# Performance work log

Measured on AMD Instinct MI355X. Metric: run time of the kernel, lower is better.

Reference implementation:

```python
import jax, jax.numpy as jnp
import numpy as np

LEAKY_SLOPE = 0.01

def bilinear_interpolate(grid, coords):
    # grid: [H, W, C]; coords: [N, 2] in [0,1] (x, y order as in torch code)
    H = grid.shape[0] - 1
    W = grid.shape[1] - 1
    fx = coords[:, 0] * W
    fy = coords[:, 1] * H
    x0 = fx.astype(jnp.int32)
    y0 = fy.astype(jnp.int32)
    xf = jnp.mod(fx, 1.0)
    yf = jnp.mod(fy, 1.0)
    x1 = jnp.minimum(x0 + 1, W)
    y1 = jnp.minimum(y0 + 1, H)
    tl = grid[y0, x0]  # [N, C]
    tr = grid[y0, x1]
    bl = grid[y1, x0]
    br = grid[y1, x1]
    xf = xf[:, None]
    yf = yf[:, None]
    top = (1.0 - xf) * tl + xf * tr
    bot = (1.0 - xf) * bl + xf * br
    return (1.0 - yf) * top + yf * bot


def setup_inputs() -> dict:
    key = jax.random.key(0)
    ks = jax.random.split(key, 10)
    N = 2097152
    pos = jax.random.uniform(ks[0], (N, 2), dtype=jnp.float32)
    dir = jax.random.uniform(ks[1], (N, 2), dtype=jnp.float32)
    pos_grid = jax.random.normal(ks[2], (256, 256, 3), dtype=jnp.float32) * 10.0
    dir_grid = jax.random.normal(ks[3], (256, 256, 3), dtype=jnp.float32) * 10.0
    # Linear layers: PyTorch default init U(-1/sqrt(fan_in), 1/sqrt(fan_in))
    def linear(kw, kb, fan_in, fan_out):
        bound = 1.0 / np.sqrt(fan_in)
        W = jax.random.uniform(kw, (fan_out, fan_in), minval=-bound, maxval=bound, dtype=jnp.float32)
        b = jax.random.uniform(kb, (fan_out,), minval=-bound, maxval=bound, dtype=jnp.float32)
        return W, b
    W1, b1 = linear(ks[4], ks[5], 6, 64)
    W2, b2 = linear(ks[6], ks[7], 64, 64)
    W3, b3 = linear(ks[8], ks[9], 64, 1)
    return {"pos": pos, "dir": dir, "pos_grid": pos_grid, "dir_grid": dir_grid,
            "W1": W1, "b1": b1, "W2": W2, "b2": b2, "W3": W3, "b3": b3}


def reference(pos, dir, pos_grid, dir_grid, W1, b1, W2, b2, W3, b3):
    pos_feat = jax.lax.stop_gradient(bilinear_interpolate(pos_grid, pos))  # .detach() in torch
    dir_feat = jax.lax.stop_gradient(bilinear_interpolate(dir_grid, dir))
    x = jnp.concatenate([pos_feat, dir_feat], axis=1)  # [N, 6]
    x = jax.nn.leaky_relu(x @ W1.T + b1, LEAKY_SLOPE)
    x = jax.nn.leaky_relu(x @ W2.T + b2, LEAKY_SLOPE)
    return jax.nn.sigmoid(x @ W3.T + b3)  # [N, 1]
```

## Files before the change

### kernel.cpp

```cpp
#include <hip/hip_runtime.h>
#include <hip/hip_bf16.h>
#include <math.h>


#define NTHREADS 256
#define NB 4
#define LSTRIDE 72
#define WAVE_L (64 * LSTRIDE)

typedef __attribute__((ext_vector_type(8))) short bf16x8;
typedef __attribute__((ext_vector_type(4))) float f32x4;
typedef __attribute__((ext_vector_type(4))) int i32x4;
typedef __attribute__((ext_vector_type(2))) int i32x2;

static __device__ __forceinline__ short f2bf(float f) {
    return __builtin_bit_cast(short, __float2bfloat16(f));
}
static __device__ __forceinline__ int pk2(float lo, float hi) {
    unsigned short l = (unsigned short)f2bf(lo);
    unsigned short h = (unsigned short)f2bf(hi);
    return (int)(((unsigned int)h << 16) | (unsigned int)l);
}
static __device__ __forceinline__ float bflo(int u) {
    return __builtin_bit_cast(float, u << 16);
}
static __device__ __forceinline__ float bfhi(int u) {
    return __builtin_bit_cast(float, (int)(u & 0xffff0000));
}

__global__ __launch_bounds__(256) void make_patches(
    const float* __restrict__ g, int* __restrict__ pout) {
    int id = blockIdx.x * 256 + threadIdx.x;
    int y0 = id >> 8, x0 = id & 255;
    int x1 = min(x0 + 1, 255), y1 = min(y0 + 1, 255);
    const float* tl = g + (y0 * 256 + x0) * 3;
    const float* tr = g + (y0 * 256 + x1) * 3;
    const float* bl = g + (y1 * 256 + x0) * 3;
    const float* br = g + (y1 * 256 + x1) * 3;
    i32x4 u0;
    i32x2 u1;
    u0[0] = pk2(tl[0], bl[0]);
    u0[1] = pk2(tl[1], bl[1]);
    u0[2] = pk2(tl[2], bl[2]);
    u0[3] = pk2(tr[0], br[0]);
    u1[0] = pk2(tr[1], br[1]);
    u1[1] = pk2(tr[2], br[2]);
    *(i32x4*)(pout + id * 8) = u0;
    *(i32x2*)(pout + id * 8 + 4) = u1;
}

static __device__ __forceinline__ void patch_issue(
    const int* __restrict__ tab, float px, float py, int* P, float& xf,
    float& yf) {
    float fx = px * 255.0f;
    float fy = py * 255.0f;
    int x0 = (int)fx;
    int y0 = (int)fy;
    xf = fx - floorf(fx);
    yf = fy - floorf(fy);
    int idx = (y0 << 8) | x0;
    i32x4 a = *(const i32x4*)(tab + idx * 8);
    i32x2 b = *(const i32x2*)(tab + idx * 8 + 4);
    P[0] = a[0]; P[1] = a[1]; P[2] = a[2];
    P[3] = a[3]; P[4] = b[0]; P[5] = b[1];
}

static __device__ __forceinline__ void patch_lerp(const int* P, float xf,
                                                  float yf, float* f) {
#pragma unroll
    for (int ch = 0; ch < 3; ++ch) {
        float tl = bflo(P[ch]), bl = bfhi(P[ch]);
        float tr = bflo(P[ch + 3]), br = bfhi(P[ch + 3]);
        float top = fmaf(xf, tr - tl, tl);
        float bot = fmaf(xf, br - bl, bl);
        f[ch] = fmaf(yf, bot - top, top);
    }
}

__global__ __launch_bounds__(NTHREADS, 3) void mlp_mfma_kernel(
    const float* __restrict__ pos, const float* __restrict__ dir,
    const int* __restrict__ patP, const int* __restrict__ patD,
    const float* __restrict__ W1, const float* __restrict__ b1,
    const float* __restrict__ W2, const float* __restrict__ b2,
    const float* __restrict__ W3, const float* __restrict__ b3,
    float* __restrict__ out) {
    __shared__ short lds_L[4 * WAVE_L];
    __shared__ int lds_F[4 * 2 * 64 * 4];

    const int w = threadIdx.x >> 6;
    const int lane = threadIdx.x & 63;
    const int c = lane & 15;
    const int q = lane >> 4;

    short* L = lds_L + w * WAVE_L;
    int* FB = lds_F + w * (2 * 64 * 4);

    bf16x8 A1f[4];
#pragma unroll
    for (int mt = 0; mt < 4; ++mt) {
        int f = mt * 16 + c;
        bf16x8 t;
#pragma unroll
        for (int j = 0; j < 8; ++j) {
            float v = 0.0f;
            if (q == 0) {
                if (j < 6) v = W1[f * 6 + j];
                else if (j == 6) v = b1[f];
            }
            t[j] = f2bf(v);
        }
        A1f[mt] = t;
    }
    bf16x8 A2f[2][4];
#pragma unroll
    for (int kt = 0; kt < 2; ++kt)
#pragma unroll
        for (int mt = 0; mt < 4; ++mt) {
            int n2 = mt * 16 + c;
            int k0 = kt * 32 + q * 8;
            bf16x8 t;
#pragma unroll
            for (int j = 0; j < 8; ++j) t[j] = f2bf(W2[n2 * 64 + k0 + j]);
            A2f[kt][mt] = t;
        }
    f32x4 ci[4], w3q[4];
#pragma unroll
    for (int ft = 0; ft < 4; ++ft)
#pragma unroll
        for (int r = 0; r < 4; ++r) {
            ci[ft][r] = b2[ft * 16 + q * 4 + r];
            w3q[ft][r] = W3[ft * 16 + q * 4 + r];
        }
    const float b3s = b3[0];
    const int dbias = pk2(1.0f, 0.0f);

    const long wave_global = (long)blockIdx.x * 4 + w;
    const long base0 = wave_global * (64L * NB);
    const f32x4 zacc = {0.f, 0.f, 0.f, 0.f};
    const float2* pos2 = (const float2*)pos;
    const float2* dir2 = (const float2*)dir;

    int PA[12], PB[12];
    float frA[4], frB[4];
    float2 cp2, cd2, cp3, cd3;

    {
        float2 c0p = pos2[base0 + lane], c0d = dir2[base0 + lane];
        float2 c1p = pos2[base0 + 64 + lane], c1d = dir2[base0 + 64 + lane];
        cp2 = pos2[base0 + 128 + lane];
        cd2 = dir2[base0 + 128 + lane];
        cp3 = pos2[base0 + 192 + lane];
        cd3 = dir2[base0 + 192 + lane];
        int P0_[12];
        float fr0[4];
        patch_issue(patP, c0p.x, c0p.y, P0_, fr0[0], fr0[1]);
        patch_issue(patD, c0d.x, c0d.y, P0_ + 6, fr0[2], fr0[3]);
        float feat[6];
        patch_lerp(P0_, fr0[0], fr0[1], feat);
        patch_lerp(P0_ + 6, fr0[2], fr0[3], feat + 3);
        i32x4 dv;
        dv[0] = pk2(feat[0], feat[1]);
        dv[1] = pk2(feat[2], feat[3]);
        dv[2] = pk2(feat[4], feat[5]);
        dv[3] = dbias;
        *(i32x4*)(FB + lane * 4) = dv;
        patch_issue(patP, c1p.x, c1p.y, PA, frA[0], frA[1]);
        patch_issue(patD, c1d.x, c1d.y, PA + 6, frA[2], frA[3]);
    }

#pragma unroll 1
    for (int ib = 0; ib < NB; ++ib) {
        const long base = base0 + ib * 64;
        const int cur = ib & 1;

        patch_issue(patP, cp2.x, cp2.y, PB, frB[0], frB[1]);
        patch_issue(patD, cd2.x, cd2.y, PB + 6, frB[2], frB[3]);

        {
            float feat[6];
            patch_lerp(PA, frA[0], frA[1], feat);
            patch_lerp(PA + 6, frA[2], frA[3], feat + 3);
            i32x4 dv;
            dv[0] = pk2(feat[0], feat[1]);
            dv[1] = pk2(feat[2], feat[3]);
            dv[2] = pk2(feat[4], feat[5]);
            dv[3] = dbias;
            *(i32x4*)(FB + (cur ^ 1) * 256 + lane * 4) = dv;
        }

#pragma unroll
        for (int pt = 0; pt < 4; ++pt) {
            const int row = pt * 16 + c;
            i32x4 bi = *(const i32x4*)(FB + cur * 256 + row * 4);
            bf16x8 bfrag = __builtin_bit_cast(bf16x8, bi);
            f32x4 a1[4];
#pragma unroll
            for (int mt = 0; mt < 4; ++mt)
                a1[mt] = __builtin_amdgcn_mfma_f32_16x16x32_bf16(
                    A1f[mt], bfrag, zacc, 0, 0, 0);
#pragma unroll
            for (int mt = 0; mt < 4; ++mt) {
                float l0 = a1[mt][0], l1 = a1[mt][1];
                float l2 = a1[mt][2], l3 = a1[mt][3];
                l0 = fmaxf(l0, 0.01f * l0);
                l1 = fmaxf(l1, 0.01f * l1);
                l2 = fmaxf(l2, 0.01f * l2);
                l3 = fmaxf(l3, 0.01f * l3);
                i32x2 wv;
                wv[0] = pk2(l0, l1);
                wv[1] = pk2(l2, l3);
                *(i32x2*)(L + row * LSTRIDE + mt * 16 + q * 4) = wv;
            }
        }

        float s[4];
#pragma unroll
        for (int pt = 0; pt < 4; ++pt) {
            const int row = pt * 16 + c;
            bf16x8 h0 = *(const bf16x8*)(L + row * LSTRIDE + q * 8);
            bf16x8 h1 = *(const bf16x8*)(L + row * LSTRIDE + 32 + q * 8);
            float t = 0.0f;
#pragma unroll
            for (int ft = 0; ft < 4; ++ft) {
                f32x4 t0 = __builtin_amdgcn_mfma_f32_16x16x32_bf16(
                    A2f[0][ft], h0, ci[ft], 0, 0, 0);
                f32x4 a2 = __builtin_amdgcn_mfma_f32_16x16x32_bf16(
                    A2f[1][ft], h1, t0, 0, 0, 0);
#pragma unroll
                for (int r = 0; r < 4; ++r) {
                    float x = a2[r];
                    x = fmaxf(x, 0.01f * x);
                    t = fmaf(x, w3q[ft][r], t);
                }
            }
            t += __shfl_xor(t, 16, 64);
            t += __shfl_xor(t, 32, 64);
            s[pt] = t;
        }

        float sa = (q & 1) ? s[1] : s[0];
        float sb = (q & 1) ? s[3] : s[2];
        float v = (q & 2) ? sb : sa;
        v += b3s;
        v = 1.0f / (1.0f + __expf(-v));
        out[base + q * 16 + c] = v;

#pragma unroll
        for (int i2 = 0; i2 < 12; ++i2) PA[i2] = PB[i2];
        frA[0] = frB[0]; frA[1] = frB[1]; frA[2] = frB[2]; frA[3] = frB[3];
        cp2 = cp3;
        cd2 = cd3;
        int mb = min(ib + 4, NB - 1);
        cp3 = pos2[base0 + mb * 64 + lane];
        cd3 = dir2[base0 + mb * 64 + lane];
    }
}

extern "C" void kernel_launch(void* const* d_in, const int* in_sizes, int n_in,
                              void* d_out, int out_size, void* d_ws,
                              size_t ws_size, hipStream_t stream) {
    const float* pos = (const float*)d_in[0];
    const float* dir = (const float*)d_in[1];
    const float* pos_grid = (const float*)d_in[2];
    const float* dir_grid = (const float*)d_in[3];
    const float* W1 = (const float*)d_in[4];
    const float* b1 = (const float*)d_in[5];
    const float* W2 = (const float*)d_in[6];
    const float* b2 = (const float*)d_in[7];
    const float* W3 = (const float*)d_in[8];
    const float* b3 = (const float*)d_in[9];
    float* out = (float*)d_out;

    int* patP = (int*)d_ws;
    int* patD = patP + 65536 * 8;

    make_patches<<<256, 256, 0, stream>>>(pos_grid, patP);
    make_patches<<<256, 256, 0, stream>>>(dir_grid, patD);

    const int n = in_sizes[0] / 2;
    const int batches = n / 64;
    const int waves = batches / NB;
    const int blocks = waves / 4;

    mlp_mfma_kernel<<<blocks, NTHREADS, 0, stream>>>(
        pos, dir, patP, patD, W1, b1, W2, b2, W3, b3, out);
}
```

Before: 160.7 us.

## Chain MLP layers in registers via 16x16x16 MFMA and drop LDS hidden buffer

Switches from 16x16x32 to 16x16x16 bf16 MFMA so the layer-1 output fragment layout matches the layer-2 B operand. Hidden activations can then be converted to bf16 in registers instead of round-tripping through a per-wave LDS buffer. It also removes the large LDS allocation, raises the occupancy hint from 3 to 4 blocks, shortens the coordinate prefetch depth, and merges the two patch-building launches into one. The risk is twice as many MFMA instructions for layer 2, plus padding waste in layer 1.

```diff
diff --git a/kernel.cpp b/kernel.cpp
--- a/kernel.cpp
+++ b/kernel.cpp
@@ -5,10 +5,8 @@
 
 #define NTHREADS 256
 #define NB 4
-#define LSTRIDE 72
-#define WAVE_L (64 * LSTRIDE)
-
-typedef __attribute__((ext_vector_type(8))) short bf16x8;
+
+typedef __attribute__((ext_vector_type(4))) short s16x4;
 typedef __attribute__((ext_vector_type(4))) float f32x4;
 typedef __attribute__((ext_vector_type(4))) int i32x4;
 typedef __attribute__((ext_vector_type(2))) int i32x2;
@@ -29,8 +27,12 @@
 }
 
 __global__ __launch_bounds__(256) void make_patches(
-    const float* __restrict__ g, int* __restrict__ pout) {
-    int id = blockIdx.x * 256 + threadIdx.x;
+    const float* __restrict__ gP, const float* __restrict__ gD,
+    int* __restrict__ outP, int* __restrict__ outD) {
+    int gid = blockIdx.x * 256 + threadIdx.x;
+    const float* g = (gid < 65536) ? gP : gD;
+    int* po = (gid < 65536) ? outP : outD;
+    int id = gid & 65535;
     int y0 = id >> 8, x0 = id & 255;
     int x1 = min(x0 + 1, 255), y1 = min(y0 + 1, 255);
     const float* tl = g + (y0 * 256 + x0) * 3;
@@ -45,8 +47,8 @@
     u0[3] = pk2(tr[0], br[0]);
     u1[0] = pk2(tr[1], br[1]);
     u1[1] = pk2(tr[2], br[2]);
-    *(i32x4*)(pout + id * 8) = u0;
-    *(i32x2*)(pout + id * 8 + 4) = u1;
+    *(i32x4*)(po + id * 8) = u0;
+    *(i32x2*)(po + id * 8 + 4) = u1;
 }
 
 static __device__ __forceinline__ void patch_issue(
@@ -77,14 +79,13 @@
     }
 }
 
-__global__ __launch_bounds__(NTHREADS, 3) void mlp_mfma_kernel(
+__global__ __launch_bounds__(NTHREADS, 4) void mlp_mfma_kernel(
     const float* __restrict__ pos, const float* __restrict__ dir,
     const int* __restrict__ patP, const int* __restrict__ patD,
     const float* __restrict__ W1, const float* __restrict__ b1,
     const float* __restrict__ W2, const float* __restrict__ b2,
     const float* __restrict__ W3, const float* __restrict__ b3,
     float* __restrict__ out) {
-    __shared__ short lds_L[4 * WAVE_L];
     __shared__ int lds_F[4 * 2 * 64 * 4];
 
     const int w = threadIdx.x >> 6;
@@ -92,65 +93,61 @@
     const int c = lane & 15;
     const int q = lane >> 4;
 
-    short* L = lds_L + w * WAVE_L;
     int* FB = lds_F + w * (2 * 64 * 4);
 
-    bf16x8 A1f[4];
+    s16x4 A1f[4];
 #pragma unroll
     for (int mt = 0; mt < 4; ++mt) {
         int f = mt * 16 + c;
-        bf16x8 t;
-#pragma unroll
-        for (int j = 0; j < 8; ++j) {
+        s16x4 t;
+#pragma unroll
+        for (int j = 0; j < 4; ++j) {
+            int k = q * 4 + j;
             float v = 0.0f;
-            if (q == 0) {
-                if (j < 6) v = W1[f * 6 + j];
-                else if (j == 6) v = b1[f];
-            }
+            if (k < 6) v = W1[f * 6 + k];
+            else if (k == 6) v = b1[f];
             t[j] = f2bf(v);
         }
         A1f[mt] = t;
     }
-    bf16x8 A2f[2][4];
-#pragma unroll
-    for (int kt = 0; kt < 2; ++kt)
+    s16x4 A2f[4][4];
+#pragma unroll
+    for (int kt = 0; kt < 4; ++kt)
 #pragma unroll
         for (int mt = 0; mt < 4; ++mt) {
             int n2 = mt * 16 + c;
-            int k0 = kt * 32 + q * 8;
-            bf16x8 t;
-#pragma unroll
-            for (int j = 0; j < 8; ++j) t[j] = f2bf(W2[n2 * 64 + k0 + j]);
+            int k0 = kt * 16 + q * 4;
+            s16x4 t;
+#pragma unroll
+            for (int j = 0; j < 4; ++j) t[j] = f2bf(W2[n2 * 64 + k0 + j]);
             A2f[kt][mt] = t;
         }
     f32x4 ci[4], w3q[4];
 #pragma unroll
-    for (int ft = 0; ft < 4; ++ft)
+    for (int mt = 0; mt < 4; ++mt)
 #pragma unroll
         for (int r = 0; r < 4; ++r) {
-            ci[ft][r] = b2[ft * 16 + q * 4 + r];
-            w3q[ft][r] = W3[ft * 16 + q * 4 + r];
+            ci[mt][r] = b2[mt * 16 + q * 4 + r];
+            w3q[mt][r] = W3[mt * 16 + q * 4 + r];
         }
     const float b3s = b3[0];
     const int dbias = pk2(1.0f, 0.0f);
+    const f32x4 zacc = {0.f, 0.f, 0.f, 0.f};
 
     const long wave_global = (long)blockIdx.x * 4 + w;
     const long base0 = wave_global * (64L * NB);
-    const f32x4 zacc = {0.f, 0.f, 0.f, 0.f};
     const float2* pos2 = (const float2*)pos;
     const float2* dir2 = (const float2*)dir;
 
-    int PA[12], PB[12];
-    float frA[4], frB[4];
-    float2 cp2, cd2, cp3, cd3;
+    int PA[12];
+    float frA[4];
+    float2 cpn, cdn;
 
     {
         float2 c0p = pos2[base0 + lane], c0d = dir2[base0 + lane];
         float2 c1p = pos2[base0 + 64 + lane], c1d = dir2[base0 + 64 + lane];
-        cp2 = pos2[base0 + 128 + lane];
-        cd2 = dir2[base0 + 128 + lane];
-        cp3 = pos2[base0 + 192 + lane];
-        cd3 = dir2[base0 + 192 + lane];
+        cpn = pos2[base0 + 128 + lane];
+        cdn = dir2[base0 + 128 + lane];
         int P0_[12];
         float fr0[4];
         patch_issue(patP, c0p.x, c0p.y, P0_, fr0[0], fr0[1]);
@@ -173,8 +170,10 @@
         const long base = base0 + ib * 64;
         const int cur = ib & 1;
 
-        patch_issue(patP, cp2.x, cp2.y, PB, frB[0], frB[1]);
-        patch_issue(patD, cd2.x, cd2.y, PB + 6, frB[2], frB[3]);
+        int PB[12];
+        float frB[4];
+        patch_issue(patP, cpn.x, cpn.y, PB, frB[0], frB[1]);
+        patch_issue(patD, cdn.x, cdn.y, PB + 6, frB[2], frB[3]);
 
         {
             float feat[6];
@@ -188,54 +187,53 @@
             *(i32x4*)(FB + (cur ^ 1) * 256 + lane * 4) = dv;
         }
 
-#pragma unroll
-        for (int pt = 0; pt < 4; ++pt) {
-            const int row = pt * 16 + c;
-            i32x4 bi = *(const i32x4*)(FB + cur * 256 + row * 4);
-            bf16x8 bfrag = __builtin_bit_cast(bf16x8, bi);
+        float s[4];
+#pragma unroll
+        for (int t = 0; t < 4; ++t) {
+            i32x2 bi = *(const i32x2*)(FB + cur * 256 + (t * 16 + c) * 4 +
+                                       (q & 1) * 2);
+            s16x4 bfeat = __builtin_bit_cast(s16x4, bi);
+
             f32x4 a1[4];
 #pragma unroll
             for (int mt = 0; mt < 4; ++mt)
-                a1[mt] = __builtin_amdgcn_mfma_f32_16x16x32_bf16(
-                    A1f[mt], bfrag, zacc, 0, 0, 0);
-#pragma unroll
-            for (int mt = 0; mt < 4; ++mt) {
-                float l0 = a1[mt][0], l1 = a1[mt][1];
-                float l2 = a1[mt][2], l3 = a1[mt][3];
-                l0 = fmaxf(l0, 0.01f * l0);
-                l1 = fmaxf(l1, 0.01f * l1);
-                l2 = fmaxf(l2, 0.01f * l2);
-                l3 = fmaxf(l3, 0.01f * l3);
-                i32x2 wv;
-                wv[0] = pk2(l0, l1);
-                wv[1] = pk2(l2, l3);
-                *(i32x2*)(L + row * LSTRIDE + mt * 16 + q * 4) = wv;
+                a1[mt] = __builtin_amdgcn_mfma_f32_16x16x16bf16_1k(
+                    A1f[mt], bfeat, zacc, 0, 0, 0);
+
+            s16x4 bh[4];
+#pragma unroll
+            for (int kt = 0; kt < 4; ++kt) {
+                s16x4 hv;
+#pragma unroll
+                for (int r = 0; r < 4; ++r) {
+                    float x = a1[kt][r];
+                    hv[r] = f2bf(fmaxf(x, 0.01f * x));
+                }
+                bh[kt] = hv;
             }
-        }
-
-        float s[4];
-#pragma unroll
-        for (int pt = 0; pt < 4; ++pt) {
-            const int row = pt * 16 + c;
-            bf16x8 h0 = *(const bf16x8*)(L + row * LSTRIDE + q * 8);
-            bf16x8 h1 = *(const bf16x8*)(L + row * LSTRIDE + 32 + q * 8);
-            float t = 0.0f;
-#pragma unroll
-            for (int ft = 0; ft < 4; ++ft) {
-                f32x4 t0 = __builtin_amdgcn_mfma_f32_16x16x32_bf16(
-                    A2f[0][ft], h0, ci[ft], 0, 0, 0);
-                f32x4 a2 = __builtin_amdgcn_mfma_f32_16x16x32_bf16(
-                    A2f[1][ft], h1, t0, 0, 0, 0);
+
+            f32x4 a2[4];
+#pragma unroll
+            for (int mt = 0; mt < 4; ++mt) a2[mt] = ci[mt];
+#pragma unroll
+            for (int kt = 0; kt < 4; ++kt)
+#pragma unroll
+                for (int mt = 0; mt < 4; ++mt)
+                    a2[mt] = __builtin_amdgcn_mfma_f32_16x16x16bf16_1k(
+                        A2f[kt][mt], bh[kt], a2[mt], 0, 0, 0);
+
+            float tt = 0.0f;
+#pragma unroll
+            for (int mt = 0; mt < 4; ++mt)
 #pragma unroll
                 for (int r = 0; r < 4; ++r) {
-                    float x = a2[r];
+                    float x = a2[mt][r];
                     x = fmaxf(x, 0.01f * x);
-                    t = fmaf(x, w3q[ft][r], t);
+                    tt = fmaf(x, w3q[mt][r], tt);
                 }
-            }
-            t += __shfl_xor(t, 16, 64);
-            t += __shfl_xor(t, 32, 64);
-            s[pt] = t;
+            tt += __shfl_xor(tt, 16, 64);
+            tt += __shfl_xor(tt, 32, 64);
+            s[t] = tt;
         }
 
         float sa = (q & 1) ? s[1] : s[0];
@@ -248,11 +246,9 @@
 #pragma unroll
         for (int i2 = 0; i2 < 12; ++i2) PA[i2] = PB[i2];
         frA[0] = frB[0]; frA[1] = frB[1]; frA[2] = frB[2]; frA[3] = frB[3];
-        cp2 = cp3;
-        cd2 = cd3;
-        int mb = min(ib + 4, NB - 1);
-        cp3 = pos2[base0 + mb * 64 + lane];
-        cd3 = dir2[base0 + mb * 64 + lane];
+        int mb = min(ib + 3, NB - 1);
+        cpn = pos2[base0 + mb * 64 + lane];
+        cdn = dir2[base0 + mb * 64 + lane];
     }
 }
 
@@ -274,8 +270,7 @@
     int* patP = (int*)d_ws;
     int* patD = patP + 65536 * 8;
 
-    make_patches<<<256, 256, 0, stream>>>(pos_grid, patP);
-    make_patches<<<256, 256, 0, stream>>>(dir_grid, patD);
+    make_patches<<<512, 256, 0, stream>>>(pos_grid, dir_grid, patP, patD);
 
     const int n = in_sizes[0] / 2;
     const int batches = n / 64;
```

New measurement: 183.5 us. 14.2% more time.
